# Optimization experiments

Hardware: AMD Instinct MI355X
Metric: run time of the kernel (lower is better)

The kernel has to match this reference:

```python
import jax, jax.numpy as jnp
import numpy as np

N = 100_000      # nodes
E = 1_600_000    # edges (avg degree 16)
IN = 128         # in_features
F = 64           # out_features
H = 1            # num_heads (module's broadcasting only valid for H==1)
S = 1            # num_samples
SLOPE = 0.2      # leaky relu negative slope


def setup_inputs() -> dict:
    key = jax.random.key(0)
    ks = jax.random.split(key, 6)
    feat = jax.random.normal(ks[0], (N, IN), jnp.float32)
    src = jax.random.randint(ks[1], (E,), 0, N)
    dst = jax.random.randint(ks[2], (E,), 0, N)
    noise = jax.random.normal(ks[3], (E, S, H, 1), jnp.float32)  # rsample noise
    W_fc = jax.random.normal(ks[4], (IN, H * F), jnp.float32) / np.sqrt(IN)
    W_post = jax.random.normal(ks[5], (F, 4), jnp.float32) / np.sqrt(F)
    b_post = jnp.zeros((4,), jnp.float32)
    bias = jnp.zeros((H, F), jnp.float32)
    return dict(feat=feat, W_fc=W_fc, W_post=W_post, b_post=b_post,
                bias=bias, noise=noise, src=src, dst=dst)


def reference(feat, W_fc, W_post, b_post, bias, noise, src, dst):
    # node projection: [N, IN] -> [N, H, F]
    h = (feat @ W_fc).reshape(N, H, F)
    # posterior params: [N, H, 4] -> four [N, H, 1]
    pp = h @ W_post + b_post
    loc_l, loc_r, lsl, lsr = jnp.split(pp, 4, axis=-1)
    # per-edge u_add_v gathers
    loc_e = loc_l[src] + loc_r[dst]                       # [E, H, 1]
    loc_e = jnp.where(loc_e >= 0, loc_e, SLOPE * loc_e)   # leaky relu
    scale_e = jnp.exp(lsl[src] + lsr[dst])                # [E, H, 1]
    # reparameterized sample: [E, S, H, 1]
    e = loc_e[:, None] + scale_e[:, None] * noise
    # edge softmax over incoming edges of each dst node
    emax = jax.ops.segment_max(e, dst, num_segments=N)
    e_exp = jnp.exp(e - emax[dst])
    esum = jax.ops.segment_sum(e_exp, dst, num_segments=N)
    a = e_exp / esum[dst]                                 # [E, S, H, 1]
    a = jnp.swapaxes(a, 1, -1)                            # [E, 1, H, S]
    # u_mul_e then scatter-sum to dst: [E, H, F, 1] * [E, 1, H, S]
    m = h[src][..., None] * a                             # [E, H, F, S] (H==1)
    rst = jax.ops.segment_sum(m, dst, num_segments=N)     # [N, H, F, S]
    return rst + bias[..., None]
```

## Files before the change

kernel.cpp:

```cpp
#include <hip/hip_runtime.h>
#include <math.h>

#define NSLOPE 0.2f
#define ASTRIDE 136
#define NPART 8
#define CAPP 208
#define CSTR 16

typedef __attribute__((ext_vector_type(8))) short bf16x8;
typedef __attribute__((ext_vector_type(4))) short bf16x4;
typedef __attribute__((ext_vector_type(4))) float f32x4;

__device__ __forceinline__ unsigned short f2bf(float x) {
    unsigned u = __float_as_uint(x);
    u += 0x7fffu + ((u >> 16) & 1u);
    return (unsigned short)(u >> 16);
}

__global__ __launch_bounds__(256) void z0_zero(int* __restrict__ bcnt, int nctr) {
    int i = blockIdx.x * 256 + threadIdx.x;
    if (i < nctr) bcnt[i * CSTR] = 0;
}

__global__ __launch_bounds__(128) void kW(const float* __restrict__ wfc,
                                          const float* __restrict__ wpost,
                                          float4* __restrict__ wc) {
    __shared__ float wp_s[256];
    int t = threadIdx.x;
    wp_s[t] = wpost[t];
    wp_s[128 + t] = wpost[128 + t];
    __syncthreads();
    float a0 = 0.f, a1 = 0.f, a2 = 0.f, a3 = 0.f;
    for (int n = 0; n < 64; n++) {
        float w = wfc[t * 64 + n];
        a0 += w * wp_s[n * 4 + 0]; a1 += w * wp_s[n * 4 + 1];
        a2 += w * wp_s[n * 4 + 2]; a3 += w * wp_s[n * 4 + 3];
    }
    float4 o; o.x = a0; o.y = a1; o.z = a2; o.w = a3;
    wc[t] = o;
}

__global__ __launch_bounds__(256) void k1_mfma(
    const float* __restrict__ feat, const float* __restrict__ wfc,
    float4* __restrict__ h_g, int n)
{
    __shared__ unsigned short a_s[64 * ASTRIDE];
    __shared__ unsigned short b_s[64 * ASTRIDE];
    int t = threadIdx.x;
    int row0 = blockIdx.x * 64;
    for (int i = t; i < 2048; i += 256) {
        int row = i >> 5, c4 = (i & 31) * 4;
        float4 f = {0.f, 0.f, 0.f, 0.f};
        if (row0 + row < n) f = ((const float4*)(feat + (long)(row0 + row) * 128))[i & 31];
        bf16x4 b4;
        b4.x = (short)f2bf(f.x); b4.y = (short)f2bf(f.y);
        b4.z = (short)f2bf(f.z); b4.w = (short)f2bf(f.w);
        *(bf16x4*)(a_s + row * ASTRIDE + c4) = b4;
    }
    for (int i = t; i < 2048; i += 256) {
        int k = i >> 4, n0 = (i & 15) * 4;
        float4 f = ((const float4*)wfc)[i];
        b_s[(n0 + 0) * ASTRIDE + k] = f2bf(f.x);
        b_s[(n0 + 1) * ASTRIDE + k] = f2bf(f.y);
        b_s[(n0 + 2) * ASTRIDE + k] = f2bf(f.z);
        b_s[(n0 + 3) * ASTRIDE + k] = f2bf(f.w);
    }
    __syncthreads();
    int lane = t & 63, wv = t >> 6;
    int c = lane & 15, quad = lane >> 4;
    f32x4 acc[4] = {{0.f,0.f,0.f,0.f},{0.f,0.f,0.f,0.f},{0.f,0.f,0.f,0.f},{0.f,0.f,0.f,0.f}};
    int arow = wv * 16 + c;
    #pragma unroll
    for (int kb = 0; kb < 4; kb++) {
        int ko = kb * 32 + quad * 8;
        bf16x8 af = *(const bf16x8*)(a_s + arow * ASTRIDE + ko);
        #pragma unroll
        for (int tt = 0; tt < 4; tt++) {
            bf16x8 bf = *(const bf16x8*)(b_s + (tt * 16 + c) * ASTRIDE + ko);
            acc[tt] = __builtin_amdgcn_mfma_f32_16x16x32_bf16(af, bf, acc[tt], 0, 0, 0);
        }
    }
    __syncthreads();
    unsigned short* h_s = a_s;
    #pragma unroll
    for (int tt = 0; tt < 4; tt++)
        #pragma unroll
        for (int r = 0; r < 4; r++)
            h_s[(wv * 16 + quad * 4 + r) * 64 + tt * 16 + c] = f2bf(acc[tt][r]);
    __syncthreads();
    for (int i = t; i < 512; i += 256) {
        int row = i >> 3;
        if (row0 + row < n)
            h_g[(long)(row0 + row) * 8 + (i & 7)] = *(const float4*)(h_s + row * 64 + (i & 7) * 8);
    }
}

__global__ __launch_bounds__(256) void k1b_pp(
    const float* __restrict__ feat, const float4* __restrict__ wc,
    const float* __restrict__ bpost, float4* __restrict__ pp, int N)
{
    int wid = (int)((blockIdx.x * 256 + threadIdx.x) >> 6);
    int lane = threadIdx.x & 63;
    if (wid >= N) return;
    const float* fr = feat + (long)wid * 128;
    float f0 = fr[lane], f1 = fr[64 + lane];
    float4 w0 = wc[lane], w1 = wc[64 + lane];
    float p0 = f0 * w0.x + f1 * w1.x;
    float p1 = f0 * w0.y + f1 * w1.y;
    float p2 = f0 * w0.z + f1 * w1.z;
    float p3 = f0 * w0.w + f1 * w1.w;
    #pragma unroll
    for (int off = 1; off < 64; off <<= 1) {
        p0 += __shfl_xor(p0, off);
        p1 += __shfl_xor(p1, off);
        p2 += __shfl_xor(p2, off);
        p3 += __shfl_xor(p3, off);
    }
    if (lane == 0) {
        float4 bp = *((const float4*)bpost);
        float4 o;
        o.x = p0 + bp.x; o.y = p1 + bp.y; o.z = p2 + bp.z; o.w = p3 + bp.w;
        pp[wid] = o;
    }
}

__global__ __launch_bounds__(256) void k4_scatter(
    const int* __restrict__ src, const int* __restrict__ dst,
    const float* __restrict__ noise, const float4* __restrict__ pp,
    int* __restrict__ bcnt, float2* __restrict__ ed, int E)
{
    int e = blockIdx.x * 256 + threadIdx.x;
    int part = blockIdx.x & (NPART - 1);
    if (e >= E) return;
    int s = __builtin_nontemporal_load(src + e);
    int d = __builtin_nontemporal_load(dst + e);
    float4 ps = pp[s], pd = pp[d];
    float loc = ps.x + pd.y;
    loc = loc >= 0.f ? loc : NSLOPE * loc;
    float ev = loc + __expf(ps.z + pd.w) * __builtin_nontemporal_load(noise + e);
    int bp = (d >> 6) * NPART + part;
    int rk = atomicAdd(&bcnt[bp * CSTR], 1);
    if (rk < CAPP) {
        float2 v; v.x = ev;
        v.y = __uint_as_float((unsigned)s | ((unsigned)(d & 63) << 26));
        ed[(long)bp * CAPP + rk] = v;
    }
}

__global__ __launch_bounds__(256) void k56_node(
    const int* __restrict__ bcnt, const float2* __restrict__ ed,
    const uint4* __restrict__ h8, const float* __restrict__ bias,
    float4* __restrict__ out4, int N)
{
    __shared__ float    s_ev[NPART * CAPP];
    __shared__ unsigned s_pk[NPART * CAPP];
    __shared__ float    o_ev[NPART * CAPP + 8];
    __shared__ unsigned o_sr[NPART * CAPP + 8];
    __shared__ int c[64], ox[64], c2[64];
    __shared__ int pcnt[NPART], pbase[NPART + 1];
    int t = threadIdx.x;
    int b = blockIdx.x;
    int n0 = b << 6;
    if (t < 64) { c[t] = 0; c2[t] = 0; }
    if (t < NPART) {
        int v = bcnt[(b * NPART + t) * CSTR];
        pcnt[t] = v < CAPP ? v : CAPP;
    }
    __syncthreads();
    if (t == 0) {
        int run = 0;
        #pragma unroll
        for (int p = 0; p < NPART; p++) { pbase[p] = run; run += pcnt[p]; }
        pbase[NPART] = run;
    }
    __syncthreads();
    int tot = pbase[NPART];
    for (int p = 0; p < NPART; p++) {
        int base = pbase[p], np = pcnt[p];
        const float2* rp = ed + (long)(b * NPART + p) * CAPP;
        for (int i = t; i < np; i += 256) {
            float2 v = rp[i];
            unsigned pk = __float_as_uint(v.y);
            s_ev[base + i] = v.x;
            s_pk[base + i] = pk;
            atomicAdd(&c[pk >> 26], 1);
        }
    }
    __syncthreads();
    if (t < 64) {
        int val = c[t], inc = val;
        #pragma unroll
        for (int off = 1; off < 64; off <<= 1) {
            int u = __shfl_up(inc, off);
            if (t >= off) inc += u;
        }
        ox[t] = inc - val;
    }
    __syncthreads();
    for (int i = t; i < tot; i += 256) {
        unsigned pk = s_pk[i];
        int dl = pk >> 26;
        int p = ox[dl] + atomicAdd(&c2[dl], 1);
        o_ev[p] = s_ev[i];
        o_sr[p] = pk & 0x03FFFFFFu;
    }
    __syncthreads();
    if (t < 64 && c[t] > 0) {
        int i0 = ox[t], i1 = i0 + c[t];
        float m = -INFINITY;
        for (int i = i0; i < i1; i++) m = fmaxf(m, o_ev[i]);
        float ssum = 0.f;
        for (int i = i0; i < i1; i++) { float w = __expf(o_ev[i] - m); o_ev[i] = w; ssum += w; }
        float inv = 1.f / ssum;
        for (int i = i0; i < i1; i++) o_ev[i] *= inv;
    }
    __syncthreads();
    int lane = t & 63, wv = t >> 6;
    int ch = lane & 7, sub = lane >> 3;
    for (int r = 0; r < 16; r++) {
        int nn = wv * 16 + r;
        int node = n0 + nn;
        int cntn = (node < N) ? c[nn] : 0;
        int i0 = ox[nn];
        float a[8] = {0.f,0.f,0.f,0.f,0.f,0.f,0.f,0.f};
        int jb = 0;
        for (; jb + 16 <= cntn; jb += 16) {
            int j0 = i0 + jb + sub, j1 = j0 + 8;
            float w0 = o_ev[j0]; int s0 = (int)o_sr[j0];
            float w1 = o_ev[j1]; int s1 = (int)o_sr[j1];
            uint4 p0 = h8[(long)s0 * 8 + ch];
            uint4 p1 = h8[(long)s1 * 8 + ch];
            a[0] += w0 * __uint_as_float(p0.x << 16);
            a[1] += w0 * __uint_as_float(p0.x & 0xffff0000u);
            a[2] += w0 * __uint_as_float(p0.y << 16);
            a[3] += w0 * __uint_as_float(p0.y & 0xffff0000u);
            a[4] += w0 * __uint_as_float(p0.z << 16);
            a[5] += w0 * __uint_as_float(p0.z & 0xffff0000u);
            a[6] += w0 * __uint_as_float(p0.w << 16);
            a[7] += w0 * __uint_as_float(p0.w & 0xffff0000u);
            a[0] += w1 * __uint_as_float(p1.x << 16);
            a[1] += w1 * __uint_as_float(p1.x & 0xffff0000u);
            a[2] += w1 * __uint_as_float(p1.y << 16);
            a[3] += w1 * __uint_as_float(p1.y & 0xffff0000u);
            a[4] += w1 * __uint_as_float(p1.z << 16);
            a[5] += w1 * __uint_as_float(p1.z & 0xffff0000u);
            a[6] += w1 * __uint_as_float(p1.w << 16);
            a[7] += w1 * __uint_as_float(p1.w & 0xffff0000u);
        }
        for (; jb < cntn; jb += 8) {
            bool vld = (jb + sub) < cntn;
            int jj = vld ? (i0 + jb + sub) : 0;
            float wv2 = vld ? o_ev[jj] : 0.f;
            int   sv  = vld ? (int)o_sr[jj] : 0;
            uint4 p = h8[(long)sv * 8 + ch];
            a[0] += wv2 * __uint_as_float(p.x << 16);
            a[1] += wv2 * __uint_as_float(p.x & 0xffff0000u);
            a[2] += wv2 * __uint_as_float(p.y << 16);
            a[3] += wv2 * __uint_as_float(p.y & 0xffff0000u);
            a[4] += wv2 * __uint_as_float(p.z << 16);
            a[5] += wv2 * __uint_as_float(p.z & 0xffff0000u);
            a[6] += wv2 * __uint_as_float(p.w << 16);
            a[7] += wv2 * __uint_as_float(p.w & 0xffff0000u);
        }
        #pragma unroll
        for (int off = 8; off < 64; off <<= 1)
            #pragma unroll
            for (int i = 0; i < 8; i++) a[i] += __shfl_xor(a[i], off);
        if (sub == 0 && node < N) {
            f32x4 o0, o1;
            const float* bl = bias + ch * 8;
            o0[0] = a[0] + bl[0]; o0[1] = a[1] + bl[1]; o0[2] = a[2] + bl[2]; o0[3] = a[3] + bl[3];
            o1[0] = a[4] + bl[4]; o1[1] = a[5] + bl[5]; o1[2] = a[6] + bl[6]; o1[3] = a[7] + bl[7];
            __builtin_nontemporal_store(o0, (f32x4*)(out4 + (long)node * 16 + ch * 2));
            __builtin_nontemporal_store(o1, (f32x4*)(out4 + (long)node * 16 + ch * 2 + 1));
        }
    }
}

extern "C" void kernel_launch(void* const* d_in, const int* in_sizes, int n_in,
                              void* d_out, int out_size, void* d_ws, size_t ws_size,
                              hipStream_t stream) {
    const float* feat  = (const float*)d_in[0];
    const float* wfc   = (const float*)d_in[1];
    const float* wpost = (const float*)d_in[2];
    const float* bpost = (const float*)d_in[3];
    const float* bias  = (const float*)d_in[4];
    const float* noise = (const float*)d_in[5];
    const int*   src   = (const int*)d_in[6];
    const int*   dst   = (const int*)d_in[7];
    int N = in_sizes[0] / 128;
    int E = in_sizes[6];
    int NB = (N + 63) / 64;
    int nctr = NB * NPART;

    float*  ws   = (float*)d_ws;
    float2* ed   = (float2*)ws;
    float*  h    = ws + (size_t)2 * NB * NPART * CAPP;
    float4* pp   = (float4*)(h + (size_t)32 * N);
    int*    bcnt = (int*)(h + (size_t)32 * N + (size_t)4 * N);
    float4* wc   = (float4*)(bcnt + (size_t)nctr * CSTR);

    hipLaunchKernelGGL(z0_zero, dim3((nctr + 255) / 256), dim3(256), 0, stream, bcnt, nctr);
    hipLaunchKernelGGL(kW, dim3(1), dim3(128), 0, stream, wfc, wpost, wc);
    hipLaunchKernelGGL(k1_mfma, dim3((N + 63) / 64), dim3(256), 0, stream,
                       feat, wfc, (float4*)h, N);
    hipLaunchKernelGGL(k1b_pp, dim3((N + 3) / 4), dim3(256), 0, stream,
                       feat, wc, bpost, pp, N);
    hipLaunchKernelGGL(k4_scatter, dim3((E + 255) / 256), dim3(256), 0, stream,
                       src, dst, noise, pp, bcnt, ed, E);
    hipLaunchKernelGGL(k56_node, dim3(NB), dim3(256), 0, stream,
                       bcnt, ed, (const uint4*)h, bias, (float4*)d_out, N);
}
```

Measured before the change: 299.4 us.

## Defer edge logit computation from scatter pass into node kernel via edge indices

The scatter kernel now bins only the edge index plus local destination (4 bytes per edge) instead of computing the logit and writing an 8-byte record. The node kernel then gathers src, noise and pp per binned edge to compute the logit itself. This halves the binned buffer traffic and lets the scatter pass skip the src, noise and pp reads, at the cost of random gathers of src and noise in the node kernel. Edge indices must fit in 26 bits, which holds for 1.6M edges.

```diff
diff --git a/kernel.cpp b/kernel.cpp
--- a/kernel.cpp
+++ b/kernel.cpp
@@ -125,30 +125,23 @@
 }
 
 __global__ __launch_bounds__(256) void k4_scatter(
-    const int* __restrict__ src, const int* __restrict__ dst,
-    const float* __restrict__ noise, const float4* __restrict__ pp,
-    int* __restrict__ bcnt, float2* __restrict__ ed, int E)
+    const int* __restrict__ dst, int* __restrict__ bcnt,
+    unsigned* __restrict__ ed, int E)
 {
     int e = blockIdx.x * 256 + threadIdx.x;
     int part = blockIdx.x & (NPART - 1);
     if (e >= E) return;
-    int s = __builtin_nontemporal_load(src + e);
     int d = __builtin_nontemporal_load(dst + e);
-    float4 ps = pp[s], pd = pp[d];
-    float loc = ps.x + pd.y;
-    loc = loc >= 0.f ? loc : NSLOPE * loc;
-    float ev = loc + __expf(ps.z + pd.w) * __builtin_nontemporal_load(noise + e);
     int bp = (d >> 6) * NPART + part;
     int rk = atomicAdd(&bcnt[bp * CSTR], 1);
-    if (rk < CAPP) {
-        float2 v; v.x = ev;
-        v.y = __uint_as_float((unsigned)s | ((unsigned)(d & 63) << 26));
-        ed[(long)bp * CAPP + rk] = v;
-    }
+    if (rk < CAPP)
+        ed[(long)bp * CAPP + rk] = (unsigned)e | ((unsigned)(d & 63) << 26);
 }
 
 __global__ __launch_bounds__(256) void k56_node(
-    const int* __restrict__ bcnt, const float2* __restrict__ ed,
+    const int* __restrict__ bcnt, const unsigned* __restrict__ edb,
+    const int* __restrict__ src, const float* __restrict__ noise,
+    const float4* __restrict__ pp,
     const uint4* __restrict__ h8, const float* __restrict__ bias,
     float4* __restrict__ out4, int N)
 {
@@ -177,13 +170,19 @@
     int tot = pbase[NPART];
     for (int p = 0; p < NPART; p++) {
         int base = pbase[p], np = pcnt[p];
-        const float2* rp = ed + (long)(b * NPART + p) * CAPP;
+        const unsigned* rp = edb + (long)(b * NPART + p) * CAPP;
         for (int i = t; i < np; i += 256) {
-            float2 v = rp[i];
-            unsigned pk = __float_as_uint(v.y);
-            s_ev[base + i] = v.x;
-            s_pk[base + i] = pk;
-            atomicAdd(&c[pk >> 26], 1);
+            unsigned pk = rp[i];
+            int e  = (int)(pk & 0x03FFFFFFu);
+            int dl = (int)(pk >> 26);
+            int s  = src[e];
+            float4 ps = pp[s], pd = pp[n0 + dl];
+            float loc = ps.x + pd.y;
+            loc = loc >= 0.f ? loc : NSLOPE * loc;
+            float ev = loc + __expf(ps.z + pd.w) * noise[e];
+            s_ev[base + i] = ev;
+            s_pk[base + i] = (unsigned)s | ((unsigned)dl << 26);
+            atomicAdd(&c[dl], 1);
         }
     }
     __syncthreads();
@@ -292,13 +291,14 @@
     int E = in_sizes[6];
     int NB = (N + 63) / 64;
     int nctr = NB * NPART;
-
-    float*  ws   = (float*)d_ws;
-    float2* ed   = (float2*)ws;
-    float*  h    = ws + (size_t)2 * NB * NPART * CAPP;
-    float4* pp   = (float4*)(h + (size_t)32 * N);
-    int*    bcnt = (int*)(h + (size_t)32 * N + (size_t)4 * N);
-    float4* wc   = (float4*)(bcnt + (size_t)nctr * CSTR);
+    size_t edn = (size_t)NB * NPART * CAPP;
+
+    float*    ws   = (float*)d_ws;
+    unsigned* ed   = (unsigned*)ws;
+    float*    h    = ws + edn;
+    float4*   pp   = (float4*)(h + (size_t)32 * N);
+    int*      bcnt = (int*)(h + (size_t)32 * N + (size_t)4 * N);
+    float4*   wc   = (float4*)(bcnt + (size_t)nctr * CSTR);
 
     hipLaunchKernelGGL(z0_zero, dim3((nctr + 255) / 256), dim3(256), 0, stream, bcnt, nctr);
     hipLaunchKernelGGL(kW, dim3(1), dim3(128), 0, stream, wfc, wpost, wc);
@@ -307,7 +307,7 @@
     hipLaunchKernelGGL(k1b_pp, dim3((N + 3) / 4), dim3(256), 0, stream,
                        feat, wc, bpost, pp, N);
     hipLaunchKernelGGL(k4_scatter, dim3((E + 255) / 256), dim3(256), 0, stream,
-                       src, dst, noise, pp, bcnt, ed, E);
+                       dst, bcnt, ed, E);
     hipLaunchKernelGGL(k56_node, dim3(NB), dim3(256), 0, stream,
-                       bcnt, ed, (const uint4*)h, bias, (float4*)d_out, N);
-}
+                       bcnt, ed, src, noise, pp, (const uint4*)h, bias, (float4*)d_out, N);
+}
```

After: 319.5 us. 1.07x slower.

## Fold counter zeroing into pp kernel and drop LDS staging in node kernel

Applied to the files above, without the earlier changes.

The separate zeroing kernel for the bucket counters is removed, and that zeroing now happens at the start of k1b_pp, which saves one launch. In k56_node the edge records are no longer staged in shared memory. They are read from global memory twice: once to count per-node degrees and once to place them into sorted order. This removes about 13 KB of LDS per block and one barrier, which can allow more blocks per CU, at the cost of a second global read of the bucket data (likely served from L2).

```diff
diff --git a/kernel.cpp b/kernel.cpp
--- a/kernel.cpp
+++ b/kernel.cpp
@@ -15,11 +15,6 @@
     unsigned u = __float_as_uint(x);
     u += 0x7fffu + ((u >> 16) & 1u);
     return (unsigned short)(u >> 16);
-}
-
-__global__ __launch_bounds__(256) void z0_zero(int* __restrict__ bcnt, int nctr) {
-    int i = blockIdx.x * 256 + threadIdx.x;
-    if (i < nctr) bcnt[i * CSTR] = 0;
 }
 
 __global__ __launch_bounds__(128) void kW(const float* __restrict__ wfc,
@@ -97,9 +92,12 @@
 
 __global__ __launch_bounds__(256) void k1b_pp(
     const float* __restrict__ feat, const float4* __restrict__ wc,
-    const float* __restrict__ bpost, float4* __restrict__ pp, int N)
+    const float* __restrict__ bpost, float4* __restrict__ pp,
+    int* __restrict__ bcnt, int nctr, int N)
 {
-    int wid = (int)((blockIdx.x * 256 + threadIdx.x) >> 6);
+    int gid = blockIdx.x * 256 + threadIdx.x;
+    if (gid < nctr) bcnt[gid * CSTR] = 0;
+    int wid = gid >> 6;
     int lane = threadIdx.x & 63;
     if (wid >= N) return;
     const float* fr = feat + (long)wid * 128;
@@ -152,12 +150,10 @@
     const uint4* __restrict__ h8, const float* __restrict__ bias,
     float4* __restrict__ out4, int N)
 {
-    __shared__ float    s_ev[NPART * CAPP];
-    __shared__ unsigned s_pk[NPART * CAPP];
     __shared__ float    o_ev[NPART * CAPP + 8];
     __shared__ unsigned o_sr[NPART * CAPP + 8];
     __shared__ int c[64], ox[64], c2[64];
-    __shared__ int pcnt[NPART], pbase[NPART + 1];
+    __shared__ int pcnt[NPART];
     int t = threadIdx.x;
     int b = blockIdx.x;
     int n0 = b << 6;
@@ -167,24 +163,11 @@
         pcnt[t] = v < CAPP ? v : CAPP;
     }
     __syncthreads();
-    if (t == 0) {
-        int run = 0;
-        #pragma unroll
-        for (int p = 0; p < NPART; p++) { pbase[p] = run; run += pcnt[p]; }
-        pbase[NPART] = run;
-    }
-    __syncthreads();
-    int tot = pbase[NPART];
     for (int p = 0; p < NPART; p++) {
-        int base = pbase[p], np = pcnt[p];
+        int np = pcnt[p];
         const float2* rp = ed + (long)(b * NPART + p) * CAPP;
-        for (int i = t; i < np; i += 256) {
-            float2 v = rp[i];
-            unsigned pk = __float_as_uint(v.y);
-            s_ev[base + i] = v.x;
-            s_pk[base + i] = pk;
-            atomicAdd(&c[pk >> 26], 1);
-        }
+        for (int i = t; i < np; i += 256)
+            atomicAdd(&c[__float_as_uint(rp[i].y) >> 26], 1);
     }
     __syncthreads();
     if (t < 64) {
@@ -197,12 +180,17 @@
         ox[t] = inc - val;
     }
     __syncthreads();
-    for (int i = t; i < tot; i += 256) {
-        unsigned pk = s_pk[i];
-        int dl = pk >> 26;
-        int p = ox[dl] + atomicAdd(&c2[dl], 1);
-        o_ev[p] = s_ev[i];
-        o_sr[p] = pk & 0x03FFFFFFu;
+    for (int p = 0; p < NPART; p++) {
+        int np = pcnt[p];
+        const float2* rp = ed + (long)(b * NPART + p) * CAPP;
+        for (int i = t; i < np; i += 256) {
+            float2 v = rp[i];
+            unsigned pk = __float_as_uint(v.y);
+            int dl = pk >> 26;
+            int pos = ox[dl] + atomicAdd(&c2[dl], 1);
+            o_ev[pos] = v.x;
+            o_sr[pos] = pk & 0x03FFFFFFu;
+        }
     }
     __syncthreads();
     if (t < 64 && c[t] > 0) {
@@ -300,12 +288,11 @@
     int*    bcnt = (int*)(h + (size_t)32 * N + (size_t)4 * N);
     float4* wc   = (float4*)(bcnt + (size_t)nctr * CSTR);
 
-    hipLaunchKernelGGL(z0_zero, dim3((nctr + 255) / 256), dim3(256), 0, stream, bcnt, nctr);
     hipLaunchKernelGGL(kW, dim3(1), dim3(128), 0, stream, wfc, wpost, wc);
     hipLaunchKernelGGL(k1_mfma, dim3((N + 63) / 64), dim3(256), 0, stream,
                        feat, wfc, (float4*)h, N);
     hipLaunchKernelGGL(k1b_pp, dim3((N + 3) / 4), dim3(256), 0, stream,
-                       feat, wc, bpost, pp, N);
+                       feat, wc, bpost, pp, bcnt, nctr, N);
     hipLaunchKernelGGL(k4_scatter, dim3((E + 255) / 256), dim3(256), 0, stream,
                        src, dst, noise, pp, bcnt, ed, E);
     hipLaunchKernelGGL(k56_node, dim3(NB), dim3(256), 0, stream,
```

Result: faster. 279.0 us (-6.8%).
